# Performance work log

Measured on AMD Instinct MI355X. Metric: run time of the kernel, lower is better.

The kernel has to match this reference:

```python
import jax, jax.numpy as jnp
from jax import lax
import numpy as np

B, T, N, F_IN, H, E, K = 8, 32, 500, 64, 128, 8000, 3
LN_EPS = 1e-5


def setup_inputs() -> dict:
    key = jax.random.key(0)
    ks = jax.random.split(key, 10)
    x = jax.random.normal(ks[0], (B, T, N, F_IN), dtype=jnp.float32)
    edge_index = jax.random.randint(ks[1], (2, E), 0, N, dtype=jnp.int64)
    edge_weight = jax.random.uniform(ks[2], (E,), dtype=jnp.float32)
    # GCNConv: linear (in->out) + bias
    W_gcn = jax.random.normal(ks[3], (F_IN, H), dtype=jnp.float32) / np.sqrt(F_IN)
    b_gcn = jnp.zeros((H,), dtype=jnp.float32)
    # Conv1d(H, H, K): weight (O, I, K)
    W_temp = jax.random.normal(ks[4], (H, H, K), dtype=jnp.float32) / np.sqrt(H * K)
    b_temp = jnp.zeros((H,), dtype=jnp.float32)
    # LayerNorm(H)
    ln_w = jnp.ones((H,), dtype=jnp.float32)
    ln_b = jnp.zeros((H,), dtype=jnp.float32)
    # residual Linear (in->out)
    W_res = jax.random.normal(ks[5], (F_IN, H), dtype=jnp.float32) / np.sqrt(F_IN)
    b_res = jnp.zeros((H,), dtype=jnp.float32)
    return {"x": x, "edge_index": edge_index, "edge_weight": edge_weight,
            "W_gcn": W_gcn, "b_gcn": b_gcn, "W_temp": W_temp, "b_temp": b_temp,
            "ln_w": ln_w, "ln_b": ln_b, "W_res": W_res, "b_res": b_res}


def reference(x, edge_index, edge_weight, W_gcn, b_gcn, W_temp, b_temp, ln_w, ln_b, W_res, b_res):
    Bv, Tv, Nv, Fv = x.shape
    Hv = W_gcn.shape[1]
    res = x @ W_res + b_res  # (B,T,N,H)

    # ---- spatial GCNConv on B*T replicated graphs (vectorized, no index offsetting) ----
    xf = x.reshape(Bv * Tv, Nv, Fv) @ W_gcn  # (BT,N,H)
    src, dst = edge_index[0], edge_index[1]
    loops = jnp.arange(Nv, dtype=edge_index.dtype)
    src2 = jnp.concatenate([src, loops])
    dst2 = jnp.concatenate([dst, loops])
    ew2 = jnp.concatenate([edge_weight, jnp.ones((Nv,), dtype=edge_weight.dtype)])
    deg = jax.ops.segment_sum(ew2, dst2, num_segments=Nv)
    dinv = jnp.where(deg > 0, deg ** -0.5, 0.0)
    norm = dinv[src2] * ew2 * dinv[dst2]  # (E+N,)
    msgs = xf[:, src2, :] * norm[None, :, None]  # (BT, E+N, H)
    agg = jax.vmap(lambda m: jax.ops.segment_sum(m, dst2, num_segments=Nv))(msgs)
    h = jax.nn.gelu(agg + b_gcn, approximate=False)  # (BT,N,H)

    # ---- temporal Conv1d over T ----
    h = h.reshape(Bv, Tv, Nv, Hv).transpose(0, 2, 3, 1).reshape(Bv * Nv, Hv, Tv)
    pad = K // 2
    h = lax.conv_general_dilated(h, W_temp, window_strides=(1,), padding=[(pad, pad)],
                                 dimension_numbers=("NCH", "OIH", "NCH"))
    h = jax.nn.gelu(h + b_temp[None, :, None], approximate=False)
    h = h.reshape(Bv, Nv, Hv, Tv).transpose(0, 3, 1, 2)  # (B,T,N,H)

    # ---- fused residual + LayerNorm over last dim ----
    y = h + res
    mu = jnp.mean(y, axis=-1, keepdims=True)
    var = jnp.mean((y - mu) ** 2, axis=-1, keepdims=True)
    return (y - mu) * lax.rsqrt(var + LN_EPS) * ln_w + ln_b
```

## Files before the change

### kernel.cpp

```cpp
#include <hip/hip_runtime.h>
#include <hip/hip_bf16.h>
#include <math.h>

#define Bv 8
#define Tv 32
#define Nv 500
#define Fin 64
#define Hv 128
#define Ev 8000
#define Kv 3
#define BT (Bv*Tv)
#define ROWS (BT*Nv)
#define TP (Tv+2)
#define KK (Kv*Hv)
#define LDSROW 144
#define AGROW 72

typedef __attribute__((ext_vector_type(8))) short s8v;
typedef __attribute__((ext_vector_type(4))) float f4v;

__device__ __forceinline__ float gelu_exact(float v){
    float t  = v*0.70710678118654752440f;
    float ax = fabsf(t);
    float k  = __builtin_amdgcn_rcpf(fmaf(0.3275911f, ax, 1.0f));
    float p  = k*fmaf(k, fmaf(k, fmaf(k, fmaf(k, 1.061405429f, -1.453152027f),
                                      1.421413741f), -0.284496736f), 0.254829592f);
    float e  = __expf(-ax*ax);
    float er = fmaf(-p, e, 1.0f);
    er = copysignf(er, t);
    return 0.5f*v*(1.0f + er);
}
__device__ __forceinline__ short f2bs(float f){
    union { __hip_bfloat16 h; short s; } u;
    u.h = __float2bfloat16(f);
    return u.s;
}
__device__ __forceinline__ float b2f(short s){
    union { unsigned int i; float f; } u;
    u.i = ((unsigned int)(unsigned short)s) << 16;
    return u.f;
}

__global__ __launch_bounds__(1024) void k_xprep(const float* __restrict__ x,
        short* __restrict__ X2b, const float* __restrict__ W,
        const float* __restrict__ Wg, const float* __restrict__ Wr,
        short* __restrict__ W2, short* __restrict__ Wgt, short* __restrict__ Wrt,
        const int* __restrict__ ei, const float* __restrict__ ew,
        float* __restrict__ dinv, int* __restrict__ offs,
        int* __restrict__ csrc, float* __restrict__ cw){
    __shared__ float sdeg[Nv];
    __shared__ int   scnt[Nv];
    __shared__ float sdv[Nv];
    __shared__ int   scur[Nv];
    __shared__ int   sa[512], sb[512];
    int bid = blockIdx.x;
    int tid = threadIdx.x;
    if (bid == 0){
        if (tid < Nv){ sdeg[tid] = 1.0f; scnt[tid] = 0; }
        __syncthreads();
        for (int e = tid; e < Ev; e += 1024){
            int d = ei[Ev + e];
            atomicAdd(&sdeg[d], ew[e]);
            atomicAdd(&scnt[d], 1);
        }
        __syncthreads();
        int c = 0;
        if (tid < Nv){
            float d = sdeg[tid];
            float v = (d > 0.f) ? rsqrtf(d) : 0.f;
            sdv[tid] = v; dinv[tid] = v;
        }
        if (tid < 512){ c = (tid < Nv) ? scnt[tid] : 0; sa[tid] = c; }
        __syncthreads();
        int* s = sa; int* t = sb;
        for (int off = 1; off < 512; off <<= 1){
            int v = 0;
            if (tid < 512){ v = s[tid]; if (tid >= off) v += s[tid - off]; }
            if (tid < 512) t[tid] = v;
            __syncthreads();
            int* tmp = s; s = t; t = tmp;
        }
        if (tid < Nv){ int excl = s[tid] - c; offs[tid] = excl; scur[tid] = excl; }
        if (tid == 0) offs[Nv] = Ev;
        __syncthreads();
        for (int e = tid; e < Ev; e += 1024){
            int sn = ei[e], d = ei[Ev + e];
            int pos = atomicAdd(&scur[d], 1);
            csrc[pos] = sn;
            cw[pos] = sdv[sn]*ew[e]*sdv[d];
        }
    } else if (bid <= ROWS/64){
        int gid = (bid-1)*1024 + tid;
        int row = gid >> 4, c4 = gid & 15;
        int bt = row / Nv;
        int n  = row - bt*Nv;
        float4 v = ((const float4*)x)[gid];
        short4 sv;
        sv.x = f2bs(v.x); sv.y = f2bs(v.y); sv.z = f2bs(v.z); sv.w = f2bs(v.w);
        *(short4*)(X2b + (size_t)n*(BT*64) + bt*64 + c4*4) = sv;
    } else {
        int idx = (bid - 1 - ROWS/64)*1024 + tid;
        if (idx < Hv*Hv*Kv){
            int o = idx/(Hv*Kv);
            int rem = idx - o*(Hv*Kv);
            int i = rem/Kv, k = rem - i*Kv;
            W2[o*KK + k*Hv + i] = f2bs(W[idx]);
        } else if (idx < Hv*Hv*Kv + Hv*64){
            int j = idx - Hv*Hv*Kv;
            int o = j >> 6, k = j & 63;
            Wgt[j] = f2bs(Wg[k*Hv + o]);
        } else if (idx < Hv*Hv*Kv + 2*Hv*64){
            int j = idx - Hv*Hv*Kv - Hv*64;
            int o = j >> 6, k = j & 63;
            Wrt[j] = f2bs(Wr[k*Hv + o]);
        }
    }
}

__global__ __launch_bounds__(256, 2) void k_mega(
        const short* __restrict__ X2b,
        const float* __restrict__ dinv, const int* __restrict__ offs,
        const int* __restrict__ csrc, const float* __restrict__ cw,
        const short* __restrict__ W2, const short* __restrict__ Wgt,
        const short* __restrict__ Wrt,
        const float* __restrict__ bg, const float* __restrict__ btm,
        const float* __restrict__ br, const float* __restrict__ lw,
        const float* __restrict__ lb, float* __restrict__ out){
    __shared__ short hs[4*TP*LDSROW];
    __shared__ short ags[4*Tv*AGROW];
    __shared__ float red[Tv][4][2];
    int tid  = threadIdx.x;
    int w    = tid >> 6;
    int lane = tid & 63;
    int quad = lane >> 4;
    int laneo = lane & 15;
    int bid = blockIdx.x;
    int b  = bid & 7;
    int n0 = (bid >> 3) * 4;
    int o_base = w*32;

    float bgv[2], bbv[2], brv[2], lwv[2], lbv[2];
    #pragma unroll
    for (int nt = 0; nt < 2; ++nt){
        int o = o_base + nt*16 + laneo;
        bgv[nt] = bg[o]; bbv[nt] = btm[o]; brv[nt] = br[o];
        lwv[nt] = lw[o]; lbv[nt] = lb[o];
    }

    s8v bwg[2][2];
    #pragma unroll
    for (int nt = 0; nt < 2; ++nt){
        const short* wp = Wgt + (o_base + nt*16 + laneo)*64 + quad*8;
        bwg[nt][0] = *(const s8v*)wp;
        bwg[nt][1] = *(const s8v*)(wp + 32);
    }

    if (tid < 128){
        int node = tid >> 5, rem = tid & 31;
        int tp = (rem >> 4)*(TP-1), c8 = rem & 15;
        s8v z = {0,0,0,0,0,0,0,0};
        *(s8v*)&hs[node*(TP*LDSROW) + tp*LDSROW + c8*8] = z;
    }

    {
        int r  = tid >> 3;
        int c8 = tid & 7;
        int woff = b*2048 + tid*8;
        for (int g = 0; g < 4; ++g){
            int n = n0 + g;
            float dv = dinv[n];
            float sw = dv*dv;
            float acc[8];
            s8v v = *(const s8v*)(X2b + (size_t)n*(BT*64) + woff);
            #pragma unroll
            for (int q = 0; q < 8; ++q) acc[q] = sw * b2f(v[q]);
            int e0 = offs[n], e1 = offs[n+1];
            for (int e = e0; e < e1; ++e){
                int s = csrc[e]; float we = cw[e];
                s8v u = *(const s8v*)(X2b + (size_t)s*(BT*64) + woff);
                #pragma unroll
                for (int q = 0; q < 8; ++q) acc[q] = fmaf(we, b2f(u[q]), acc[q]);
            }
            s8v rr;
            #pragma unroll
            for (int q = 0; q < 8; ++q) rr[q] = f2bs(acc[q]);
            *(s8v*)&ags[g*(Tv*AGROW) + r*AGROW + c8*8] = rr;
        }
    }
    __syncthreads();

    for (int g = 0; g < 4; ++g){
        const short* ap = &ags[g*(Tv*AGROW)];
        #pragma unroll
        for (int m = 0; m < 2; ++m){
            const short* arp = ap + (m*16 + laneo)*AGROW + quad*8;
            s8v a0 = *(const s8v*)arp;
            s8v a1 = *(const s8v*)(arp + 32);
            f4v h0 = {0.f,0.f,0.f,0.f}, h1 = {0.f,0.f,0.f,0.f};
            h0 = __builtin_amdgcn_mfma_f32_16x16x32_bf16(a0, bwg[0][0], h0, 0,0,0);
            h0 = __builtin_amdgcn_mfma_f32_16x16x32_bf16(a1, bwg[0][1], h0, 0,0,0);
            h1 = __builtin_amdgcn_mfma_f32_16x16x32_bf16(a0, bwg[1][0], h1, 0,0,0);
            h1 = __builtin_amdgcn_mfma_f32_16x16x32_bf16(a1, bwg[1][1], h1, 0,0,0);
            #pragma unroll
            for (int r = 0; r < 4; ++r){
                int tp = m*16 + quad*4 + r + 1;
                short* hrow = &hs[g*(TP*LDSROW) + tp*LDSROW];
                hrow[o_base + laneo]      = f2bs(gelu_exact(h0[r] + bgv[0]));
                hrow[o_base + 16 + laneo] = f2bs(gelu_exact(h1[r] + bgv[1]));
            }
        }
    }

    s8v breg[2][12], bwr[2][2];
    #pragma unroll
    for (int nt = 0; nt < 2; ++nt){
        int o = o_base + nt*16 + laneo;
        const short* wp = W2 + o*KK + quad*8;
        #pragma unroll
        for (int s = 0; s < 12; ++s)
            breg[nt][s] = *(const s8v*)(wp + s*32);
        const short* wr = Wrt + o*64 + quad*8;
        bwr[nt][0] = *(const s8v*)wr;
        bwr[nt][1] = *(const s8v*)(wr + 32);
    }
    __syncthreads();

    for (int g = 0; g < 4; ++g){
        int n = n0 + g;
        f4v acc[2][2];
        #pragma unroll
        for (int m = 0; m < 2; ++m)
            #pragma unroll
            for (int nt = 0; nt < 2; ++nt)
                acc[m][nt] = (f4v){0.f,0.f,0.f,0.f};
        #pragma unroll
        for (int m = 0; m < 2; ++m){
            #pragma unroll
            for (int s = 0; s < 12; ++s){
                int k  = s >> 2;
                int i0 = (s & 3) * 32;
                int tp = m*16 + laneo + k;
                s8v a = *(const s8v*)&hs[g*(TP*LDSROW) + tp*LDSROW + i0 + quad*8];
                acc[m][0] = __builtin_amdgcn_mfma_f32_16x16x32_bf16(a, breg[0][s], acc[m][0], 0,0,0);
                acc[m][1] = __builtin_amdgcn_mfma_f32_16x16x32_bf16(a, breg[1][s], acc[m][1], 0,0,0);
            }
        }
        f4v racc[2][2];
        #pragma unroll
        for (int m = 0; m < 2; ++m)
            #pragma unroll
            for (int nt = 0; nt < 2; ++nt)
                racc[m][nt] = (f4v){0.f,0.f,0.f,0.f};
        const short* xp = X2b + ((size_t)n*BT + b*Tv)*64;
        #pragma unroll
        for (int m = 0; m < 2; ++m){
            const short* xrp = xp + (m*16 + laneo)*64 + quad*8;
            s8v a0 = *(const s8v*)xrp;
            s8v a1 = *(const s8v*)(xrp + 32);
            racc[m][0] = __builtin_amdgcn_mfma_f32_16x16x32_bf16(a0, bwr[0][0], racc[m][0], 0,0,0);
            racc[m][0] = __builtin_amdgcn_mfma_f32_16x16x32_bf16(a1, bwr[0][1], racc[m][0], 0,0,0);
            racc[m][1] = __builtin_amdgcn_mfma_f32_16x16x32_bf16(a0, bwr[1][0], racc[m][1], 0,0,0);
            racc[m][1] = __builtin_amdgcn_mfma_f32_16x16x32_bf16(a1, bwr[1][1], racc[m][1], 0,0,0);
        }
        size_t obase = ((size_t)b*Tv*Nv + n)*Hv;
        float yv[2][2][4];
        float srow[2][4], ssrow[2][4];
        #pragma unroll
        for (int m = 0; m < 2; ++m)
            #pragma unroll
            for (int r = 0; r < 4; ++r){ srow[m][r] = 0.f; ssrow[m][r] = 0.f; }
        #pragma unroll
        for (int m = 0; m < 2; ++m){
            #pragma unroll
            for (int nt = 0; nt < 2; ++nt){
                #pragma unroll
                for (int r = 0; r < 4; ++r){
                    float gv = gelu_exact(acc[m][nt][r] + bbv[nt]);
                    float y = gv + racc[m][nt][r] + brv[nt];
                    yv[m][nt][r] = y;
                    srow[m][r] += y; ssrow[m][r] += y*y;
                }
            }
        }
        #pragma unroll
        for (int m = 0; m < 2; ++m)
            #pragma unroll
            for (int r = 0; r < 4; ++r){
                #pragma unroll
                for (int msk = 8; msk >= 1; msk >>= 1){
                    srow[m][r]  += __shfl_xor(srow[m][r],  msk, 64);
                    ssrow[m][r] += __shfl_xor(ssrow[m][r], msk, 64);
                }
            }
        if (laneo == 0){
            #pragma unroll
            for (int m = 0; m < 2; ++m)
                #pragma unroll
                for (int r = 0; r < 4; ++r){
                    int t = m*16 + quad*4 + r;
                    red[t][w][0] = srow[m][r];
                    red[t][w][1] = ssrow[m][r];
                }
        }
        __syncthreads();
        #pragma unroll
        for (int m = 0; m < 2; ++m){
            #pragma unroll
            for (int r = 0; r < 4; ++r){
                int t = m*16 + quad*4 + r;
                float s  = red[t][0][0] + red[t][1][0] + red[t][2][0] + red[t][3][0];
                float ss = red[t][0][1] + red[t][1][1] + red[t][2][1] + red[t][3][1];
                float mu = s * (1.f/128.f);
                float var = fmaxf(ss * (1.f/128.f) - mu*mu, 0.f);
                float rstd = rsqrtf(var + 1e-5f);
                #pragma unroll
                for (int nt = 0; nt < 2; ++nt){
                    int o = o_base + nt*16 + laneo;
                    out[obase + (size_t)t*Nv*Hv + o] =
                        (yv[m][nt][r] - mu)*rstd*lwv[nt] + lbv[nt];
                }
            }
        }
        __syncthreads();
    }
}

extern "C" void kernel_launch(void* const* d_in, const int* in_sizes, int n_in,
                              void* d_out, int out_size, void* d_ws, size_t ws_size,
                              hipStream_t stream){
    const float* x   = (const float*)d_in[0];
    const int*   ei  = (const int*)d_in[1];
    const float* ew  = (const float*)d_in[2];
    const float* Wg  = (const float*)d_in[3];
    const float* bg  = (const float*)d_in[4];
    const float* Wtm = (const float*)d_in[5];
    const float* btm = (const float*)d_in[6];
    const float* lw  = (const float*)d_in[7];
    const float* lb  = (const float*)d_in[8];
    const float* Wr  = (const float*)d_in[9];
    const float* br  = (const float*)d_in[10];
    float* out = (float*)d_out;

    char* ws = (char*)d_ws;
    float* dinv = (float*)(ws + 0);
    int*   offs = (int*)  (ws + 4096);
    int*   csrc = (int*)  (ws + 8192);
    float* cwn  = (float*)(ws + 40960);
    short* W2   = (short*)(ws + 73728);
    short* Wgt  = (short*)(ws + 172032);
    short* Wrt  = (short*)(ws + 188416);
    short* X2b  = (short*)(ws + 204800);

    k_xprep<<<1 + ROWS/64 + 64, 1024, 0, stream>>>(x, X2b, Wtm, Wg, Wr,
                                                   W2, Wgt, Wrt,
                                                   ei, ew, dinv, offs, csrc, cwn);
    k_mega <<<(Bv*Nv)/4, 256, 0, stream>>>(X2b, dinv, offs, csrc, cwn,
                                           W2, Wgt, Wrt,
                                           bg, btm, br, lw, lb, out);
}
```

Before: 214.8 us.

## Keep bf16 x in natural layout, interleave 4-node gathers, shrink LDS for occupancy

The bf16 copy of x now keeps its natural (b,t,n,f) order instead of being transposed to node-major, so the conversion writes are contiguous 16-byte stores. The neighbour aggregation processes all four nodes of a block together, issuing their gathers in parallel for more memory-level parallelism. A shared zero row replaces the per-node temporal padding rows and the row pitch shrinks, cutting LDS so the launch bound can request 3 blocks per CU. The cost is that gathers in the new layout are strided by node rather than contiguous per node, plus some predicated wasted loads for nodes with fewer edges.

```diff
diff --git a/kernel.cpp b/kernel.cpp
--- a/kernel.cpp
+++ b/kernel.cpp
@@ -11,10 +11,15 @@
 #define Kv 3
 #define BT (Bv*Tv)
 #define ROWS (BT*Nv)
-#define TP (Tv+2)
 #define KK (Kv*Hv)
-#define LDSROW 144
+
+#define HROW 136
+#define HS_NODE (32*HROW)
+#define ZROW (4*HS_NODE)
+#define AGS_BASE (ZROW+HROW)
 #define AGROW 72
+#define AGS_NODE (32*AGROW)
+#define SMEM_SHORTS (AGS_BASE + 4*AGS_NODE)
 
 typedef __attribute__((ext_vector_type(8))) short s8v;
 typedef __attribute__((ext_vector_type(4))) float f4v;
@@ -42,7 +47,7 @@
 }
 
 __global__ __launch_bounds__(1024) void k_xprep(const float* __restrict__ x,
-        short* __restrict__ X2b, const float* __restrict__ W,
+        short* __restrict__ xb, const float* __restrict__ W,
         const float* __restrict__ Wg, const float* __restrict__ Wr,
         short* __restrict__ W2, short* __restrict__ Wgt, short* __restrict__ Wrt,
         const int* __restrict__ ei, const float* __restrict__ ew,
@@ -89,17 +94,17 @@
             csrc[pos] = sn;
             cw[pos] = sdv[sn]*ew[e]*sdv[d];
         }
-    } else if (bid <= ROWS/64){
+    } else if (bid <= 1000){
         int gid = (bid-1)*1024 + tid;
-        int row = gid >> 4, c4 = gid & 15;
-        int bt = row / Nv;
-        int n  = row - bt*Nv;
-        float4 v = ((const float4*)x)[gid];
-        short4 sv;
-        sv.x = f2bs(v.x); sv.y = f2bs(v.y); sv.z = f2bs(v.z); sv.w = f2bs(v.w);
-        *(short4*)(X2b + (size_t)n*(BT*64) + bt*64 + c4*4) = sv;
+        const float4* x4 = (const float4*)x;
+        float4 va = x4[gid*2];
+        float4 vb = x4[gid*2+1];
+        s8v r;
+        r[0]=f2bs(va.x); r[1]=f2bs(va.y); r[2]=f2bs(va.z); r[3]=f2bs(va.w);
+        r[4]=f2bs(vb.x); r[5]=f2bs(vb.y); r[6]=f2bs(vb.z); r[7]=f2bs(vb.w);
+        ((s8v*)xb)[gid] = r;
     } else {
-        int idx = (bid - 1 - ROWS/64)*1024 + tid;
+        int idx = (bid - 1001)*1024 + tid;
         if (idx < Hv*Hv*Kv){
             int o = idx/(Hv*Kv);
             int rem = idx - o*(Hv*Kv);
@@ -117,8 +122,8 @@
     }
 }
 
-__global__ __launch_bounds__(256, 2) void k_mega(
-        const short* __restrict__ X2b,
+__global__ __launch_bounds__(256, 3) void k_mega(
+        const short* __restrict__ xb,
         const float* __restrict__ dinv, const int* __restrict__ offs,
         const int* __restrict__ csrc, const float* __restrict__ cw,
         const short* __restrict__ W2, const short* __restrict__ Wgt,
@@ -126,9 +131,8 @@
         const float* __restrict__ bg, const float* __restrict__ btm,
         const float* __restrict__ br, const float* __restrict__ lw,
         const float* __restrict__ lb, float* __restrict__ out){
-    __shared__ short hs[4*TP*LDSROW];
-    __shared__ short ags[4*Tv*AGROW];
-    __shared__ float red[Tv][4][2];
+    __shared__ short smem[SMEM_SHORTS];
+    float (*red)[4][2] = (float(*)[4][2])&smem[AGS_BASE];
     int tid  = threadIdx.x;
     int w    = tid >> 6;
     int lane = tid & 63;
@@ -147,6 +151,58 @@
         lwv[nt] = lw[o]; lbv[nt] = lb[o];
     }
 
+    if (tid < 16){
+        s8v z = {0,0,0,0,0,0,0,0};
+        *(s8v*)&smem[ZROW + tid*8] = z;
+    }
+
+    {
+        int tr = tid >> 3;
+        int c8 = tid & 7;
+        const short* xrow = xb + ((size_t)(b*Tv + tr)*Nv)*64 + c8*8;
+        float acc[4][8];
+        int eb[4], elen[4]; int M = 0;
+        #pragma unroll
+        for (int g = 0; g < 4; ++g){
+            int n = n0 + g;
+            float dv = dinv[n];
+            float sw = dv*dv;
+            s8v v = *(const s8v*)(xrow + n*64);
+            #pragma unroll
+            for (int q = 0; q < 8; ++q) acc[g][q] = sw * b2f(v[q]);
+            eb[g] = offs[n];
+            int l = offs[n+1] - eb[g];
+            elen[g] = l;
+            M = (l > M) ? l : M;
+        }
+        for (int it = 0; it < M; ++it){
+            int sn[4]; float wv[4];
+            #pragma unroll
+            for (int g = 0; g < 4; ++g){
+                bool p = it < elen[g];
+                int idx = p ? (eb[g] + it) : 0;
+                sn[g] = csrc[idx];
+                wv[g] = p ? cw[idx] : 0.f;
+            }
+            s8v u[4];
+            #pragma unroll
+            for (int g = 0; g < 4; ++g)
+                u[g] = *(const s8v*)(xrow + sn[g]*64);
+            #pragma unroll
+            for (int g = 0; g < 4; ++g)
+                #pragma unroll
+                for (int q = 0; q < 8; ++q)
+                    acc[g][q] = fmaf(wv[g], b2f(u[g][q]), acc[g][q]);
+        }
+        #pragma unroll
+        for (int g = 0; g < 4; ++g){
+            s8v rr;
+            #pragma unroll
+            for (int q = 0; q < 8; ++q) rr[q] = f2bs(acc[g][q]);
+            *(s8v*)&smem[AGS_BASE + g*AGS_NODE + tr*AGROW + c8*8] = rr;
+        }
+    }
+
     s8v bwg[2][2];
     #pragma unroll
     for (int nt = 0; nt < 2; ++nt){
@@ -154,43 +210,10 @@
         bwg[nt][0] = *(const s8v*)wp;
         bwg[nt][1] = *(const s8v*)(wp + 32);
     }
-
-    if (tid < 128){
-        int node = tid >> 5, rem = tid & 31;
-        int tp = (rem >> 4)*(TP-1), c8 = rem & 15;
-        s8v z = {0,0,0,0,0,0,0,0};
-        *(s8v*)&hs[node*(TP*LDSROW) + tp*LDSROW + c8*8] = z;
-    }
-
-    {
-        int r  = tid >> 3;
-        int c8 = tid & 7;
-        int woff = b*2048 + tid*8;
-        for (int g = 0; g < 4; ++g){
-            int n = n0 + g;
-            float dv = dinv[n];
-            float sw = dv*dv;
-            float acc[8];
-            s8v v = *(const s8v*)(X2b + (size_t)n*(BT*64) + woff);
-            #pragma unroll
-            for (int q = 0; q < 8; ++q) acc[q] = sw * b2f(v[q]);
-            int e0 = offs[n], e1 = offs[n+1];
-            for (int e = e0; e < e1; ++e){
-                int s = csrc[e]; float we = cw[e];
-                s8v u = *(const s8v*)(X2b + (size_t)s*(BT*64) + woff);
-                #pragma unroll
-                for (int q = 0; q < 8; ++q) acc[q] = fmaf(we, b2f(u[q]), acc[q]);
-            }
-            s8v rr;
-            #pragma unroll
-            for (int q = 0; q < 8; ++q) rr[q] = f2bs(acc[q]);
-            *(s8v*)&ags[g*(Tv*AGROW) + r*AGROW + c8*8] = rr;
-        }
-    }
     __syncthreads();
 
     for (int g = 0; g < 4; ++g){
-        const short* ap = &ags[g*(Tv*AGROW)];
+        const short* ap = &smem[AGS_BASE + g*AGS_NODE];
         #pragma unroll
         for (int m = 0; m < 2; ++m){
             const short* arp = ap + (m*16 + laneo)*AGROW + quad*8;
@@ -203,8 +226,8 @@
             h1 = __builtin_amdgcn_mfma_f32_16x16x32_bf16(a1, bwg[1][1], h1, 0,0,0);
             #pragma unroll
             for (int r = 0; r < 4; ++r){
-                int tp = m*16 + quad*4 + r + 1;
-                short* hrow = &hs[g*(TP*LDSROW) + tp*LDSROW];
+                int t = m*16 + quad*4 + r;
+                short* hrow = &smem[g*HS_NODE + t*HROW];
                 hrow[o_base + laneo]      = f2bs(gelu_exact(h0[r] + bgv[0]));
                 hrow[o_base + 16 + laneo] = f2bs(gelu_exact(h1[r] + bgv[1]));
             }
@@ -239,8 +262,9 @@
             for (int s = 0; s < 12; ++s){
                 int k  = s >> 2;
                 int i0 = (s & 3) * 32;
-                int tp = m*16 + laneo + k;
-                s8v a = *(const s8v*)&hs[g*(TP*LDSROW) + tp*LDSROW + i0 + quad*8];
+                int row = m*16 + laneo + k - 1;
+                int hb = ((unsigned)row > 31u) ? ZROW : (g*HS_NODE + row*HROW);
+                s8v a = *(const s8v*)&smem[hb + i0 + quad*8];
                 acc[m][0] = __builtin_amdgcn_mfma_f32_16x16x32_bf16(a, breg[0][s], acc[m][0], 0,0,0);
                 acc[m][1] = __builtin_amdgcn_mfma_f32_16x16x32_bf16(a, breg[1][s], acc[m][1], 0,0,0);
             }
@@ -251,10 +275,9 @@
             #pragma unroll
             for (int nt = 0; nt < 2; ++nt)
                 racc[m][nt] = (f4v){0.f,0.f,0.f,0.f};
-        const short* xp = X2b + ((size_t)n*BT + b*Tv)*64;
-        #pragma unroll
-        for (int m = 0; m < 2; ++m){
-            const short* xrp = xp + (m*16 + laneo)*64 + quad*8;
+        #pragma unroll
+        for (int m = 0; m < 2; ++m){
+            const short* xrp = xb + ((size_t)(b*Tv + m*16 + laneo)*Nv + n)*64 + quad*8;
             s8v a0 = *(const s8v*)xrp;
             s8v a1 = *(const s8v*)(xrp + 32);
             racc[m][0] = __builtin_amdgcn_mfma_f32_16x16x32_bf16(a0, bwr[0][0], racc[m][0], 0,0,0);
@@ -349,12 +372,12 @@
     short* W2   = (short*)(ws + 73728);
     short* Wgt  = (short*)(ws + 172032);
     short* Wrt  = (short*)(ws + 188416);
-    short* X2b  = (short*)(ws + 204800);
-
-    k_xprep<<<1 + ROWS/64 + 64, 1024, 0, stream>>>(x, X2b, Wtm, Wg, Wr,
-                                                   W2, Wgt, Wrt,
-                                                   ei, ew, dinv, offs, csrc, cwn);
-    k_mega <<<(Bv*Nv)/4, 256, 0, stream>>>(X2b, dinv, offs, csrc, cwn,
+    short* xb   = (short*)(ws + 204800);
+
+    k_xprep<<<1 + 1000 + 64, 1024, 0, stream>>>(x, xb, Wtm, Wg, Wr,
+                                                W2, Wgt, Wrt,
+                                                ei, ew, dinv, offs, csrc, cwn);
+    k_mega <<<(Bv*Nv)/4, 256, 0, stream>>>(xb, dinv, offs, csrc, cwn,
                                            W2, Wgt, Wrt,
                                            bg, btm, br, lw, lb, out);
 }
```

Measured after the change: 237.7 us. 1.11x slower.

## Process one node per block and unroll edge gather four-wide

Applied to the files above, without the earlier changes.

The fused kernel now handles one (batch, node) pair per block instead of four nodes, launching four times as many blocks. Shared memory shrinks to a single node's buffers, temporal padding becomes a shared zero row chosen by index, and the edge aggregation loads four neighbors at once into independent accumulators. The aim is more blocks in flight and more memory-level parallelism in the gather. In exchange, each block must reload the large per-wave weight registers, so weight load traffic per node rises fourfold.

```diff
diff --git a/kernel.cpp b/kernel.cpp
--- a/kernel.cpp
+++ b/kernel.cpp
@@ -11,10 +11,13 @@
 #define Kv 3
 #define BT (Bv*Tv)
 #define ROWS (BT*Nv)
-#define TP (Tv+2)
 #define KK (Kv*Hv)
-#define LDSROW 144
+
+#define HROW 136
+#define ZROW (32*HROW)
+#define AGS_BASE (ZROW+HROW)
 #define AGROW 72
+#define SMEM_SHORTS (AGS_BASE + 32*AGROW)
 
 typedef __attribute__((ext_vector_type(8))) short s8v;
 typedef __attribute__((ext_vector_type(4))) float f4v;
@@ -126,9 +129,8 @@
         const float* __restrict__ bg, const float* __restrict__ btm,
         const float* __restrict__ br, const float* __restrict__ lw,
         const float* __restrict__ lb, float* __restrict__ out){
-    __shared__ short hs[4*TP*LDSROW];
-    __shared__ short ags[4*Tv*AGROW];
-    __shared__ float red[Tv][4][2];
+    __shared__ short smem[SMEM_SHORTS];
+    float (*red)[4][2] = (float(*)[4][2])&smem[AGS_BASE];
     int tid  = threadIdx.x;
     int w    = tid >> 6;
     int lane = tid & 63;
@@ -136,7 +138,7 @@
     int laneo = lane & 15;
     int bid = blockIdx.x;
     int b  = bid & 7;
-    int n0 = (bid >> 3) * 4;
+    int n  = bid >> 3;
     int o_base = w*32;
 
     float bgv[2], bbv[2], brv[2], lwv[2], lbv[2];
@@ -147,6 +149,51 @@
         lwv[nt] = lw[o]; lbv[nt] = lb[o];
     }
 
+    if (tid < 16){
+        s8v z = {0,0,0,0,0,0,0,0};
+        *(s8v*)&smem[ZROW + tid*8] = z;
+    }
+
+    {
+        int tr = tid >> 3;
+        int c8 = tid & 7;
+        int woff = b*2048 + tid*8;
+        float dv = dinv[n];
+        float sw = dv*dv;
+        float a4[4][8];
+        s8v v = *(const s8v*)(X2b + (size_t)n*(BT*64) + woff);
+        #pragma unroll
+        for (int q = 0; q < 8; ++q){
+            a4[0][q] = sw * b2f(v[q]);
+            a4[1][q] = 0.f; a4[2][q] = 0.f; a4[3][q] = 0.f;
+        }
+        int e0 = offs[n], e1 = offs[n+1];
+        for (int base = e0; base < e1; base += 4){
+            int sn[4]; float wv[4];
+            #pragma unroll
+            for (int j = 0; j < 4; ++j){
+                int idx = base + j;
+                bool p = idx < e1;
+                sn[j] = p ? csrc[idx] : n;
+                wv[j] = p ? cw[idx] : 0.f;
+            }
+            s8v u[4];
+            #pragma unroll
+            for (int j = 0; j < 4; ++j)
+                u[j] = *(const s8v*)(X2b + (size_t)sn[j]*(BT*64) + woff);
+            #pragma unroll
+            for (int j = 0; j < 4; ++j)
+                #pragma unroll
+                for (int q = 0; q < 8; ++q)
+                    a4[j][q] = fmaf(wv[j], b2f(u[j][q]), a4[j][q]);
+        }
+        s8v rr;
+        #pragma unroll
+        for (int q = 0; q < 8; ++q)
+            rr[q] = f2bs((a4[0][q] + a4[1][q]) + (a4[2][q] + a4[3][q]));
+        *(s8v*)&smem[AGS_BASE + tr*AGROW + c8*8] = rr;
+    }
+
     s8v bwg[2][2];
     #pragma unroll
     for (int nt = 0; nt < 2; ++nt){
@@ -154,60 +201,24 @@
         bwg[nt][0] = *(const s8v*)wp;
         bwg[nt][1] = *(const s8v*)(wp + 32);
     }
-
-    if (tid < 128){
-        int node = tid >> 5, rem = tid & 31;
-        int tp = (rem >> 4)*(TP-1), c8 = rem & 15;
-        s8v z = {0,0,0,0,0,0,0,0};
-        *(s8v*)&hs[node*(TP*LDSROW) + tp*LDSROW + c8*8] = z;
-    }
-
-    {
-        int r  = tid >> 3;
-        int c8 = tid & 7;
-        int woff = b*2048 + tid*8;
-        for (int g = 0; g < 4; ++g){
-            int n = n0 + g;
-            float dv = dinv[n];
-            float sw = dv*dv;
-            float acc[8];
-            s8v v = *(const s8v*)(X2b + (size_t)n*(BT*64) + woff);
-            #pragma unroll
-            for (int q = 0; q < 8; ++q) acc[q] = sw * b2f(v[q]);
-            int e0 = offs[n], e1 = offs[n+1];
-            for (int e = e0; e < e1; ++e){
-                int s = csrc[e]; float we = cw[e];
-                s8v u = *(const s8v*)(X2b + (size_t)s*(BT*64) + woff);
-                #pragma unroll
-                for (int q = 0; q < 8; ++q) acc[q] = fmaf(we, b2f(u[q]), acc[q]);
-            }
-            s8v rr;
-            #pragma unroll
-            for (int q = 0; q < 8; ++q) rr[q] = f2bs(acc[q]);
-            *(s8v*)&ags[g*(Tv*AGROW) + r*AGROW + c8*8] = rr;
-        }
-    }
     __syncthreads();
 
-    for (int g = 0; g < 4; ++g){
-        const short* ap = &ags[g*(Tv*AGROW)];
-        #pragma unroll
-        for (int m = 0; m < 2; ++m){
-            const short* arp = ap + (m*16 + laneo)*AGROW + quad*8;
-            s8v a0 = *(const s8v*)arp;
-            s8v a1 = *(const s8v*)(arp + 32);
-            f4v h0 = {0.f,0.f,0.f,0.f}, h1 = {0.f,0.f,0.f,0.f};
-            h0 = __builtin_amdgcn_mfma_f32_16x16x32_bf16(a0, bwg[0][0], h0, 0,0,0);
-            h0 = __builtin_amdgcn_mfma_f32_16x16x32_bf16(a1, bwg[0][1], h0, 0,0,0);
-            h1 = __builtin_amdgcn_mfma_f32_16x16x32_bf16(a0, bwg[1][0], h1, 0,0,0);
-            h1 = __builtin_amdgcn_mfma_f32_16x16x32_bf16(a1, bwg[1][1], h1, 0,0,0);
-            #pragma unroll
-            for (int r = 0; r < 4; ++r){
-                int tp = m*16 + quad*4 + r + 1;
-                short* hrow = &hs[g*(TP*LDSROW) + tp*LDSROW];
-                hrow[o_base + laneo]      = f2bs(gelu_exact(h0[r] + bgv[0]));
-                hrow[o_base + 16 + laneo] = f2bs(gelu_exact(h1[r] + bgv[1]));
-            }
+    #pragma unroll
+    for (int m = 0; m < 2; ++m){
+        const short* arp = &smem[AGS_BASE + (m*16 + laneo)*AGROW + quad*8];
+        s8v a0 = *(const s8v*)arp;
+        s8v a1 = *(const s8v*)(arp + 32);
+        f4v h0 = {0.f,0.f,0.f,0.f}, h1 = {0.f,0.f,0.f,0.f};
+        h0 = __builtin_amdgcn_mfma_f32_16x16x32_bf16(a0, bwg[0][0], h0, 0,0,0);
+        h0 = __builtin_amdgcn_mfma_f32_16x16x32_bf16(a1, bwg[0][1], h0, 0,0,0);
+        h1 = __builtin_amdgcn_mfma_f32_16x16x32_bf16(a0, bwg[1][0], h1, 0,0,0);
+        h1 = __builtin_amdgcn_mfma_f32_16x16x32_bf16(a1, bwg[1][1], h1, 0,0,0);
+        #pragma unroll
+        for (int r = 0; r < 4; ++r){
+            int t = m*16 + quad*4 + r;
+            short* hrow = &smem[t*HROW];
+            hrow[o_base + laneo]      = f2bs(gelu_exact(h0[r] + bgv[0]));
+            hrow[o_base + 16 + laneo] = f2bs(gelu_exact(h1[r] + bgv[1]));
         }
     }
 
@@ -225,103 +236,100 @@
     }
     __syncthreads();
 
-    for (int g = 0; g < 4; ++g){
-        int n = n0 + g;
-        f4v acc[2][2];
+    f4v acc[2][2];
+    #pragma unroll
+    for (int m = 0; m < 2; ++m)
+        #pragma unroll
+        for (int nt = 0; nt < 2; ++nt)
+            acc[m][nt] = (f4v){0.f,0.f,0.f,0.f};
+    #pragma unroll
+    for (int m = 0; m < 2; ++m){
+        #pragma unroll
+        for (int s = 0; s < 12; ++s){
+            int k  = s >> 2;
+            int i0 = (s & 3) * 32;
+            int row = m*16 + laneo + k - 1;
+            int hb = ((unsigned)row > 31u) ? ZROW : row*HROW;
+            s8v a = *(const s8v*)&smem[hb + i0 + quad*8];
+            acc[m][0] = __builtin_amdgcn_mfma_f32_16x16x32_bf16(a, breg[0][s], acc[m][0], 0,0,0);
+            acc[m][1] = __builtin_amdgcn_mfma_f32_16x16x32_bf16(a, breg[1][s], acc[m][1], 0,0,0);
+        }
+    }
+    f4v racc[2][2];
+    #pragma unroll
+    for (int m = 0; m < 2; ++m)
+        #pragma unroll
+        for (int nt = 0; nt < 2; ++nt)
+            racc[m][nt] = (f4v){0.f,0.f,0.f,0.f};
+    const short* xp = X2b + ((size_t)n*BT + b*Tv)*64;
+    #pragma unroll
+    for (int m = 0; m < 2; ++m){
+        const short* xrp = xp + (m*16 + laneo)*64 + quad*8;
+        s8v a0 = *(const s8v*)xrp;
+        s8v a1 = *(const s8v*)(xrp + 32);
+        racc[m][0] = __builtin_amdgcn_mfma_f32_16x16x32_bf16(a0, bwr[0][0], racc[m][0], 0,0,0);
+        racc[m][0] = __builtin_amdgcn_mfma_f32_16x16x32_bf16(a1, bwr[0][1], racc[m][0], 0,0,0);
+        racc[m][1] = __builtin_amdgcn_mfma_f32_16x16x32_bf16(a0, bwr[1][0], racc[m][1], 0,0,0);
+        racc[m][1] = __builtin_amdgcn_mfma_f32_16x16x32_bf16(a1, bwr[1][1], racc[m][1], 0,0,0);
+    }
+    size_t obase = ((size_t)b*Tv*Nv + n)*Hv;
+    float yv[2][2][4];
+    float srow[2][4], ssrow[2][4];
+    #pragma unroll
+    for (int m = 0; m < 2; ++m)
+        #pragma unroll
+        for (int r = 0; r < 4; ++r){ srow[m][r] = 0.f; ssrow[m][r] = 0.f; }
+    #pragma unroll
+    for (int m = 0; m < 2; ++m){
+        #pragma unroll
+        for (int nt = 0; nt < 2; ++nt){
+            #pragma unroll
+            for (int r = 0; r < 4; ++r){
+                float gv = gelu_exact(acc[m][nt][r] + bbv[nt]);
+                float y = gv + racc[m][nt][r] + brv[nt];
+                yv[m][nt][r] = y;
+                srow[m][r] += y; ssrow[m][r] += y*y;
+            }
+        }
+    }
+    #pragma unroll
+    for (int m = 0; m < 2; ++m)
+        #pragma unroll
+        for (int r = 0; r < 4; ++r){
+            #pragma unroll
+            for (int msk = 8; msk >= 1; msk >>= 1){
+                srow[m][r]  += __shfl_xor(srow[m][r],  msk, 64);
+                ssrow[m][r] += __shfl_xor(ssrow[m][r], msk, 64);
+            }
+        }
+    if (laneo == 0){
         #pragma unroll
         for (int m = 0; m < 2; ++m)
-            #pragma unroll
-            for (int nt = 0; nt < 2; ++nt)
-                acc[m][nt] = (f4v){0.f,0.f,0.f,0.f};
-        #pragma unroll
-        for (int m = 0; m < 2; ++m){
-            #pragma unroll
-            for (int s = 0; s < 12; ++s){
-                int k  = s >> 2;
-                int i0 = (s & 3) * 32;
-                int tp = m*16 + laneo + k;
-                s8v a = *(const s8v*)&hs[g*(TP*LDSROW) + tp*LDSROW + i0 + quad*8];
-                acc[m][0] = __builtin_amdgcn_mfma_f32_16x16x32_bf16(a, breg[0][s], acc[m][0], 0,0,0);
-                acc[m][1] = __builtin_amdgcn_mfma_f32_16x16x32_bf16(a, breg[1][s], acc[m][1], 0,0,0);
-            }
-        }
-        f4v racc[2][2];
-        #pragma unroll
-        for (int m = 0; m < 2; ++m)
-            #pragma unroll
-            for (int nt = 0; nt < 2; ++nt)
-                racc[m][nt] = (f4v){0.f,0.f,0.f,0.f};
-        const short* xp = X2b + ((size_t)n*BT + b*Tv)*64;
-        #pragma unroll
-        for (int m = 0; m < 2; ++m){
-            const short* xrp = xp + (m*16 + laneo)*64 + quad*8;
-            s8v a0 = *(const s8v*)xrp;
-            s8v a1 = *(const s8v*)(xrp + 32);
-            racc[m][0] = __builtin_amdgcn_mfma_f32_16x16x32_bf16(a0, bwr[0][0], racc[m][0], 0,0,0);
-            racc[m][0] = __builtin_amdgcn_mfma_f32_16x16x32_bf16(a1, bwr[0][1], racc[m][0], 0,0,0);
-            racc[m][1] = __builtin_amdgcn_mfma_f32_16x16x32_bf16(a0, bwr[1][0], racc[m][1], 0,0,0);
-            racc[m][1] = __builtin_amdgcn_mfma_f32_16x16x32_bf16(a1, bwr[1][1], racc[m][1], 0,0,0);
-        }
-        size_t obase = ((size_t)b*Tv*Nv + n)*Hv;
-        float yv[2][2][4];
-        float srow[2][4], ssrow[2][4];
-        #pragma unroll
-        for (int m = 0; m < 2; ++m)
-            #pragma unroll
-            for (int r = 0; r < 4; ++r){ srow[m][r] = 0.f; ssrow[m][r] = 0.f; }
-        #pragma unroll
-        for (int m = 0; m < 2; ++m){
-            #pragma unroll
-            for (int nt = 0; nt < 2; ++nt){
-                #pragma unroll
-                for (int r = 0; r < 4; ++r){
-                    float gv = gelu_exact(acc[m][nt][r] + bbv[nt]);
-                    float y = gv + racc[m][nt][r] + brv[nt];
-                    yv[m][nt][r] = y;
-                    srow[m][r] += y; ssrow[m][r] += y*y;
-                }
-            }
-        }
-        #pragma unroll
-        for (int m = 0; m < 2; ++m)
-            #pragma unroll
-            for (int r = 0; r < 4; ++r){
-                #pragma unroll
-                for (int msk = 8; msk >= 1; msk >>= 1){
-                    srow[m][r]  += __shfl_xor(srow[m][r],  msk, 64);
-                    ssrow[m][r] += __shfl_xor(ssrow[m][r], msk, 64);
-                }
-            }
-        if (laneo == 0){
-            #pragma unroll
-            for (int m = 0; m < 2; ++m)
-                #pragma unroll
-                for (int r = 0; r < 4; ++r){
-                    int t = m*16 + quad*4 + r;
-                    red[t][w][0] = srow[m][r];
-                    red[t][w][1] = ssrow[m][r];
-                }
-        }
-        __syncthreads();
-        #pragma unroll
-        for (int m = 0; m < 2; ++m){
             #pragma unroll
             for (int r = 0; r < 4; ++r){
                 int t = m*16 + quad*4 + r;
-                float s  = red[t][0][0] + red[t][1][0] + red[t][2][0] + red[t][3][0];
-                float ss = red[t][0][1] + red[t][1][1] + red[t][2][1] + red[t][3][1];
-                float mu = s * (1.f/128.f);
-                float var = fmaxf(ss * (1.f/128.f) - mu*mu, 0.f);
-                float rstd = rsqrtf(var + 1e-5f);
-                #pragma unroll
-                for (int nt = 0; nt < 2; ++nt){
-                    int o = o_base + nt*16 + laneo;
-                    out[obase + (size_t)t*Nv*Hv + o] =
-                        (yv[m][nt][r] - mu)*rstd*lwv[nt] + lbv[nt];
-                }
-            }
-        }
-        __syncthreads();
+                red[t][w][0] = srow[m][r];
+                red[t][w][1] = ssrow[m][r];
+            }
+    }
+    __syncthreads();
+    #pragma unroll
+    for (int m = 0; m < 2; ++m){
+        #pragma unroll
+        for (int r = 0; r < 4; ++r){
+            int t = m*16 + quad*4 + r;
+            float s  = red[t][0][0] + red[t][1][0] + red[t][2][0] + red[t][3][0];
+            float ss = red[t][0][1] + red[t][1][1] + red[t][2][1] + red[t][3][1];
+            float mu = s * (1.f/128.f);
+            float var = fmaxf(ss * (1.f/128.f) - mu*mu, 0.f);
+            float rstd = rsqrtf(var + 1e-5f);
+            #pragma unroll
+            for (int nt = 0; nt < 2; ++nt){
+                int o = o_base + nt*16 + laneo;
+                out[obase + (size_t)t*Nv*Hv + o] =
+                    (yv[m][nt][r] - mu)*rstd*lwv[nt] + lbv[nt];
+            }
+        }
     }
 }
 
@@ -354,7 +362,7 @@
     k_xprep<<<1 + ROWS/64 + 64, 1024, 0, stream>>>(x, X2b, Wtm, Wg, Wr,
                                                    W2, Wgt, Wrt,
                                                    ei, ew, dinv, offs, csrc, cwn);
-    k_mega <<<(Bv*Nv)/4, 256, 0, stream>>>(X2b, dinv, offs, csrc, cwn,
-                                           W2, Wgt, Wrt,
-                                           bg, btm, br, lw, lb, out);
-}
+    k_mega <<<8*Nv, 256, 0, stream>>>(X2b, dinv, offs, csrc, cwn,
+                                      W2, Wgt, Wrt,
+                                      bg, btm, br, lw, lb, out);
+}
```

Result: no change. 218.5 us (+1.7%).
